# Kernel optimization log

Hardware: AMD Instinct MI355X
Metric: run time of the kernel (lower is better)

## Reference

```python
import jax, jax.numpy as jnp
import numpy as np

D_MODEL = 1024
NUM_HEADS = 16
HEAD_DIM = D_MODEL // NUM_HEADS


def setup_inputs() -> dict:
    key = jax.random.key(0)
    ks = jax.random.split(key, 12)
    B, S = 2, 2048
    scale = 1.0 / np.sqrt(D_MODEL)
    inp = {
        "x": jax.random.normal(ks[0], (B, S, D_MODEL), dtype=jnp.float32),
        "docking_scores": jax.random.uniform(ks[1], (B, S), dtype=jnp.float32),
        "q_w": jax.random.normal(ks[2], (D_MODEL, D_MODEL), dtype=jnp.float32) * scale,
        "q_b": jnp.zeros((D_MODEL,), dtype=jnp.float32),
        "k_w": jax.random.normal(ks[3], (D_MODEL, D_MODEL), dtype=jnp.float32) * scale,
        "k_b": jnp.zeros((D_MODEL,), dtype=jnp.float32),
        "v_w": jax.random.normal(ks[4], (D_MODEL, D_MODEL), dtype=jnp.float32) * scale,
        "v_b": jnp.zeros((D_MODEL,), dtype=jnp.float32),
        "o_w": jax.random.normal(ks[5], (D_MODEL, D_MODEL), dtype=jnp.float32) * scale,
        "o_b": jnp.zeros((D_MODEL,), dtype=jnp.float32),
        "alpha": jnp.float32(0.5),
    }
    return inp


def reference(x, docking_scores, q_w, q_b, k_w, k_b, v_w, v_b, o_w, o_b, alpha):
    B, S, _ = x.shape
    # Projections; weights stored as (in, out) so y = x @ W + b
    def proj(w, b):
        y = jnp.einsum('bsd,de->bse', x, w) + b
        return y.reshape(B, S, NUM_HEADS, HEAD_DIM).transpose(0, 2, 1, 3)  # (B,H,S,hd)
    Q = proj(q_w, q_b)
    K = proj(k_w, k_b)
    V = proj(v_w, v_b)
    scores = jnp.einsum('bhqd,bhkd->bhqk', Q, K) / np.sqrt(HEAD_DIM)
    attn = jax.nn.softmax(scores, axis=-1)  # (B,H,S,S)
    # post-softmax docking blend, broadcast over heads and query positions
    ds = docking_scores[:, None, None, :]  # (B,1,1,S)
    attn = (1.0 - alpha) * attn + alpha * ds
    ctx = jnp.einsum('bhqk,bhkd->bhqd', attn, V)
    ctx = ctx.transpose(0, 2, 1, 3).reshape(B, S, D_MODEL)
    return jnp.einsum('bsd,de->bse', ctx, o_w) + o_b
```

## Files before the change

### kernel.cpp

```cpp
#include <hip/hip_runtime.h>
#include <hip/hip_bf16.h>

typedef __attribute__((ext_vector_type(8)))  short bf16x8;
typedef __attribute__((ext_vector_type(4)))  float f32x4;
typedef __attribute__((ext_vector_type(16))) float f32x16;
typedef __attribute__((ext_vector_type(4)))  int   i32x4;
typedef __attribute__((ext_vector_type(4)))  unsigned short u16x4;
typedef __attribute__((ext_vector_type(8)))  unsigned short u16x8;

__device__ __forceinline__ unsigned short f2bf(float f) {
    unsigned int u = __builtin_bit_cast(unsigned int, f);
    u += 0x7FFFu + ((u >> 16) & 1u);
    return (unsigned short)(u >> 16);
}
__device__ __forceinline__ float bf2f(unsigned short h) {
    unsigned int u = ((unsigned int)h) << 16;
    return __builtin_bit_cast(float, u);
}
__device__ __forceinline__ bf16x8 ld16(const unsigned short* p) {
    return *reinterpret_cast<const bf16x8*>(p);
}
__device__ __forceinline__ float fexp2(float x) {
    float r; asm("v_exp_f32 %0, %1" : "=v"(r) : "v"(x)); return r;
}
__device__ __forceinline__ float frcp(float x) {
    float r; asm("v_rcp_f32 %0, %1" : "=v"(r) : "v"(x)); return r;
}
__device__ __forceinline__ void pswap(unsigned int& a, unsigned int& b) {
    asm("v_permlane32_swap_b32 %0, %1" : "+v"(a), "+v"(b));
}

__global__ void cvt_x_kernel(const float* __restrict__ in, unsigned short* __restrict__ out, int n8) {
    int idx = blockIdx.x * blockDim.x + threadIdx.x;
    int stride = gridDim.x * blockDim.x;
    for (int i = idx; i < n8; i += stride) {
        f32x4 a = reinterpret_cast<const f32x4*>(in)[i*2];
        f32x4 b = reinterpret_cast<const f32x4*>(in)[i*2+1];
        u16x8 o;
        o[0]=f2bf(a[0]); o[1]=f2bf(a[1]); o[2]=f2bf(a[2]); o[3]=f2bf(a[3]);
        o[4]=f2bf(b[0]); o[5]=f2bf(b[1]); o[6]=f2bf(b[2]); o[7]=f2bf(b[3]);
        reinterpret_cast<u16x8*>(out)[i] = o;
    }
}

__global__ void tr_w_kernel(const float* __restrict__ q_w, const float* __restrict__ k_w,
                            const float* __restrict__ v_w, const float* __restrict__ o_w,
                            unsigned short* __restrict__ WT) {
    __shared__ float tile[32][33];
    const float* W = (blockIdx.z == 0) ? q_w : (blockIdx.z == 1) ? k_w : (blockIdx.z == 2) ? v_w : o_w;
    unsigned short* dst = WT + (size_t)blockIdx.z * 1024 * 1024;
    int tx = threadIdx.x, ty = threadIdx.y;
    int n0 = blockIdx.x * 32, k0 = blockIdx.y * 32;
#pragma unroll
    for (int j = 0; j < 4; ++j)
        tile[ty + j*8][tx] = W[(size_t)(k0 + ty + j*8) * 1024 + n0 + tx];
    __syncthreads();
#pragma unroll
    for (int j = 0; j < 4; ++j)
        dst[(size_t)(n0 + ty + j*8) * 1024 + k0 + tx] = f2bf(tile[tx][ty + j*8]);
}


__global__ __launch_bounds__(256) void gemm_qkv(
    const unsigned short* __restrict__ A,
    const unsigned short* __restrict__ WT,
    const float* __restrict__ qb, const float* __restrict__ kbias, const float* __restrict__ vbias,
    unsigned short* __restrict__ Qo, unsigned short* __restrict__ KFo, unsigned short* __restrict__ VFo)
{
    __shared__ __align__(16) unsigned short As[2][128*64];
    __shared__ __align__(16) unsigned short Bs[2][128*64];
    const int tid = threadIdx.x, lane = tid & 63, w = tid >> 6;
    const int wm = w >> 1, wn = w & 1;
    const int m0 = blockIdx.y * 128, n0 = blockIdx.x * 128;
    const int K = 1024;
    const int sr = tid >> 3, ssl = tid & 7;
    const int ssw = (ssl ^ (sr & 7)) << 3;
    f32x4 acc[4][4] = {};

    auto stage = [&](int buf, int k0) {
#pragma unroll
        for (int j = 0; j < 4; ++j) {
            const int c = j*256 + tid, r = j*32 + sr;
            __builtin_amdgcn_global_load_lds(
                (const __attribute__((address_space(1))) void*)&A[(size_t)(m0+r)*K + k0 + ssw],
                (__attribute__((address_space(3))) void*)&As[buf][(size_t)c*8], 16, 0, 0);
            __builtin_amdgcn_global_load_lds(
                (const __attribute__((address_space(1))) void*)&WT[(size_t)(n0+r)*K + k0 + ssw],
                (__attribute__((address_space(3))) void*)&Bs[buf][(size_t)c*8], 16, 0, 0);
        }
    };

    stage(0, 0);
#pragma unroll 1
    for (int t = 0; t < 16; ++t) {
        __syncthreads();
        if (t < 15) stage((t + 1) & 1, (t + 1) * 64);
        const unsigned short* pa = &As[t & 1][0];
        const unsigned short* pb = &Bs[t & 1][0];
#pragma unroll
        for (int kc = 0; kc < 2; ++kc) {
            bf16x8 af[4], bfr[4];
            const int slog = kc*4 + (lane >> 4);
#pragma unroll
            for (int t2 = 0; t2 < 4; ++t2) {
                const int row = wm*64 + t2*16 + (lane & 15);
                af[t2]  = ld16(&pa[row*64 + ((slog ^ (row & 7)) << 3)]);
                const int col = wn*64 + t2*16 + (lane & 15);
                bfr[t2] = ld16(&pb[col*64 + ((slog ^ (col & 7)) << 3)]);
            }
#pragma unroll
            for (int mt = 0; mt < 4; ++mt)
#pragma unroll
                for (int nt = 0; nt < 4; ++nt)
                    acc[mt][nt] = __builtin_amdgcn_mfma_f32_16x16x32_bf16(af[mt], bfr[nt], acc[mt][nt], 0, 0, 0);
        }
    }
    const int mat = n0 >> 10;
    if (mat == 2) {
#pragma unroll
        for (int mt = 0; mt < 4; ++mt)
#pragma unroll
        for (int nt = 0; nt < 4; ++nt) {
            const int nl = (n0 & 1023) + wn*64 + nt*16 + (lane & 15);
            const int h = nl >> 6, hd = nl & 63;
            const int mbase = m0 + wm*64 + mt*16 + ((lane >> 4) << 2);
            const int b = mbase >> 11, s = mbase & 2047;
            const float bv = vbias[nl];
            u16x4 pk;
#pragma unroll
            for (int r = 0; r < 4; ++r) pk[r] = f2bf(acc[mt][nt][r] + bv);
            const size_t off = (size_t)((b << 4) | h) * 131072 + (s >> 6) * 4096 + (hd >> 5) * 2048
                             + ((s >> 4) & 3) * 512 + ((s >> 3) & 1) * 256 + (hd & 31) * 8 + (s & 7);
            *reinterpret_cast<u16x4*>(&VFo[off]) = pk;
        }
    } else if (mat == 1) {
#pragma unroll
        for (int mt = 0; mt < 4; ++mt)
#pragma unroll
        for (int nt = 0; nt < 4; ++nt) {
            const int nl = (n0 & 1023) + wn*64 + nt*16 + (lane & 15);
            const int h = nl >> 6, hd = nl & 63;
            const int mbase = m0 + wm*64 + mt*16 + ((lane >> 4) << 2);
            const float bv = kbias[nl];
#pragma unroll
            for (int r = 0; r < 4; ++r) {
                const int mm2 = mbase + r, b = mm2 >> 11, s = mm2 & 2047;
                const size_t off = (size_t)((b << 4) | h) * 131072 + (s >> 5) * 2048 + (hd >> 4) * 512
                                 + ((hd >> 3) & 1) * 256 + (s & 31) * 8 + (hd & 7);
                KFo[off] = f2bf(acc[mt][nt][r] + bv);
            }
        }
    } else {
        const float scale = 0.180336881f;
#pragma unroll
        for (int mt = 0; mt < 4; ++mt)
#pragma unroll
        for (int nt = 0; nt < 4; ++nt) {
            const int nl = (n0 & 1023) + wn*64 + nt*16 + (lane & 15);
            const int h = nl >> 6, hd = nl & 63;
            const int mbase = m0 + wm*64 + mt*16 + ((lane >> 4) << 2);
            const float bv = qb[nl];
#pragma unroll
            for (int r = 0; r < 4; ++r) {
                const int mm2 = mbase + r, b = mm2 >> 11, s = mm2 & 2047;
                Qo[((size_t)((b << 4) | h) * 2048 + s) * 64 + hd] = f2bf((acc[mt][nt][r] + bv) * scale);
            }
        }
    }
}

__global__ __launch_bounds__(256) void gemm_o(
    const unsigned short* __restrict__ A, const unsigned short* __restrict__ WT,
    const float* __restrict__ bias, float* __restrict__ Cout)
{
    __shared__ __align__(16) unsigned short As[2][128*64];
    __shared__ __align__(16) unsigned short Bs[2][128*64];
    const int tid = threadIdx.x, lane = tid & 63, w = tid >> 6;
    const int wm = w >> 1, wn = w & 1;
    const int m0 = blockIdx.y * 128, n0 = blockIdx.x * 128;
    const int K = 1024;
    const int sr = tid >> 3, ssl = tid & 7;
    const int ssw = (ssl ^ (sr & 7)) << 3;
    f32x4 acc[4][4] = {};

    auto stage = [&](int buf, int k0) {
#pragma unroll
        for (int j = 0; j < 4; ++j) {
            const int c = j*256 + tid, r = j*32 + sr;
            __builtin_amdgcn_global_load_lds(
                (const __attribute__((address_space(1))) void*)&A[(size_t)(m0+r)*K + k0 + ssw],
                (__attribute__((address_space(3))) void*)&As[buf][(size_t)c*8], 16, 0, 0);
            __builtin_amdgcn_global_load_lds(
                (const __attribute__((address_space(1))) void*)&WT[(size_t)(n0+r)*K + k0 + ssw],
                (__attribute__((address_space(3))) void*)&Bs[buf][(size_t)c*8], 16, 0, 0);
        }
    };

    stage(0, 0);
#pragma unroll 1
    for (int t = 0; t < 16; ++t) {
        __syncthreads();
        if (t < 15) stage((t + 1) & 1, (t + 1) * 64);
        const unsigned short* pa = &As[t & 1][0];
        const unsigned short* pb = &Bs[t & 1][0];
#pragma unroll
        for (int kc = 0; kc < 2; ++kc) {
            bf16x8 af[4], bfr[4];
            const int slog = kc*4 + (lane >> 4);
#pragma unroll
            for (int t2 = 0; t2 < 4; ++t2) {
                const int row = wm*64 + t2*16 + (lane & 15);
                af[t2]  = ld16(&pa[row*64 + ((slog ^ (row & 7)) << 3)]);
                const int col = wn*64 + t2*16 + (lane & 15);
                bfr[t2] = ld16(&pb[col*64 + ((slog ^ (col & 7)) << 3)]);
            }
#pragma unroll
            for (int mt = 0; mt < 4; ++mt)
#pragma unroll
                for (int nt = 0; nt < 4; ++nt)
                    acc[mt][nt] = __builtin_amdgcn_mfma_f32_16x16x32_bf16(af[mt], bfr[nt], acc[mt][nt], 0, 0, 0);
        }
    }
#pragma unroll
    for (int mt = 0; mt < 4; ++mt)
#pragma unroll
    for (int nt = 0; nt < 4; ++nt) {
        const int n = n0 + wn*64 + nt*16 + (lane & 15);
        const int mbase = m0 + wm*64 + mt*16 + ((lane >> 4) << 2);
        const float bv = bias[n];
#pragma unroll
        for (int r = 0; r < 4; ++r)
            Cout[(size_t)(mbase + r) * 1024 + n] = acc[mt][nt][r] + bv;
    }
}

__global__ void dock_c_kernel(const float* __restrict__ ds, const unsigned short* __restrict__ VF,
                              float* __restrict__ cvec) {
    __shared__ float red[256];
    const int bh = blockIdx.x;
    const int b = bh >> 4;
    const int t = threadIdx.x;
    const int lane = t & 63, t2 = (t >> 6) & 1, k4 = t >> 7;
    const int hi = lane >> 5;
    const unsigned short* VFb = VF + (size_t)bh * 131072;
    const float* dsb = ds + b * 2048;
    float sum = 0.f;
    for (int kvt = k4; kvt < 32; kvt += 2) {
#pragma unroll
        for (int ks = 0; ks < 4; ++ks) {
            bf16x8 v = ld16(VFb + kvt*4096 + t2*2048 + ks*512 + lane*8);
            const int kv0 = kvt*64 + ks*16 + hi*8;
            f32x4 d0 = *reinterpret_cast<const f32x4*>(&dsb[kv0]);
            f32x4 d1 = *reinterpret_cast<const f32x4*>(&dsb[kv0 + 4]);
            sum += d0[0]*bf2f((unsigned short)v[0]) + d0[1]*bf2f((unsigned short)v[1])
                 + d0[2]*bf2f((unsigned short)v[2]) + d0[3]*bf2f((unsigned short)v[3])
                 + d1[0]*bf2f((unsigned short)v[4]) + d1[1]*bf2f((unsigned short)v[5])
                 + d1[2]*bf2f((unsigned short)v[6]) + d1[3]*bf2f((unsigned short)v[7]);
        }
    }
    red[t] = sum;
    __syncthreads();
    if (t < 64) {
        const int ln = t & 31, tt2 = t >> 5;
        const int base = tt2 * 64 + ln;
        cvec[bh * 64 + tt2 * 32 + ln] = red[base] + red[base + 32] + red[base + 128] + red[base + 160];
    }
}

__global__ __launch_bounds__(256, 2) void attn_kernel(
    const unsigned short* __restrict__ Qp,
    const unsigned short* __restrict__ KF,
    const unsigned short* __restrict__ VF,
    const float* __restrict__ cvec,
    const float* __restrict__ alpha_p,
    unsigned short* __restrict__ ctx)
{
    __shared__ float sml[4][32];
    const int tid = threadIdx.x, lane = tid & 63, w = tid >> 6;
    const int hi = lane >> 5, ln = lane & 31;
    const int wg = blockIdx.x;
    const int swz = (wg & 7) * 64 + (wg >> 3);
    const int bh = swz >> 4, qt = swz & 15;
    const int q0 = qt * 128 + w * 32;
    const size_t hb = (size_t)bh * (2048 * 64);
    const float alpha = *alpha_p;

    const unsigned short* KFb = KF + (size_t)bh * 131072;
    const unsigned short* VFb = VF + (size_t)bh * 131072;

    bf16x8 qf[4];
    {
        const unsigned short* qr = &Qp[hb + (size_t)(q0 + ln) * 64 + hi * 8];
#pragma unroll
        for (int ks = 0; ks < 4; ++ks) qf[ks] = ld16(qr + ks * 16);
    }

    const short one_bf = (short)0x3F80;
    const bf16x8 onesf = {one_bf, one_bf, one_bf, one_bf, one_bf, one_bf, one_bf, one_bf};

    f32x16 oacc0 = {}, oacc1 = {}, lacc = {};
    float m = -1e30f;

    auto ldk = [&](bf16x8 (&kf)[8], int it) {
#pragma unroll
        for (int t2 = 0; t2 < 2; ++t2)
#pragma unroll
        for (int ks = 0; ks < 4; ++ks)
            kf[t2*4+ks] = ld16(KFb + (it*2 + t2)*2048 + ks*512 + lane*8);
    };

    bf16x8 kfA[8], kfB[8];
    ldk(kfA, 0);
    f32x16 sA0 = {}, sA1 = {}, sB0 = {}, sB1 = {};
#pragma unroll
    for (int ks = 0; ks < 4; ++ks) {
        sA0 = __builtin_amdgcn_mfma_f32_32x32x16_bf16(kfA[ks],   qf[ks], sA0, 0, 0, 0);
        sA1 = __builtin_amdgcn_mfma_f32_32x32x16_bf16(kfA[4+ks], qf[ks], sA1, 0, 0, 0);
    }

    auto step = [&](f32x16& sc0, f32x16& sc1, f32x16& sn0, f32x16& sn1, bf16x8 (&kn)[8], int it) {
        bf16x8 vf[8];
#pragma unroll
        for (int t2 = 0; t2 < 2; ++t2)
#pragma unroll
        for (int ks = 0; ks < 4; ++ks)
            vf[t2*4+ks] = ld16(VFb + it*4096 + t2*2048 + ks*512 + lane*8);
        const bool more = (it + 1 < 32);
        if (more) ldk(kn, it + 1);
        float mx[8];
#pragma unroll
        for (int r = 0; r < 8; ++r)
            mx[r] = fmaxf(fmaxf(sc0[r], sc0[r+8]), fmaxf(sc1[r], sc1[r+8]));
        float tm = fmaxf(fmaxf(fmaxf(mx[0],mx[1]), fmaxf(mx[2],mx[3])),
                         fmaxf(fmaxf(mx[4],mx[5]), fmaxf(mx[6],mx[7])));
        {
            unsigned int ua = __builtin_bit_cast(unsigned int, tm), ub = ua;
            pswap(ua, ub);
            tm = fmaxf(__builtin_bit_cast(float, ua), __builtin_bit_cast(float, ub));
        }
        if (__any(tm > m + 8.f)) {
            float mn = fmaxf(m, tm);
            float sc = fexp2(m - mn);
            m = mn;
            if (hi == 0) sml[w][ln] = sc;
#pragma unroll
            for (int m4 = 0; m4 < 4; ++m4) {
                f32x4 sv = *reinterpret_cast<const f32x4*>(&sml[w][m4*8 + hi*4]);
#pragma unroll
                for (int r3 = 0; r3 < 4; ++r3) {
                    oacc0[m4*4+r3] *= sv[r3];
                    oacc1[m4*4+r3] *= sv[r3];
                    lacc [m4*4+r3] *= sv[r3];
                }
            }
        }
        float p0a[16], p1a[16];
#pragma unroll
        for (int r = 0; r < 16; ++r) {
            p0a[r] = fexp2(sc0[r] - m);
            p1a[r] = fexp2(sc1[r] - m);
        }
        unsigned int Wp0[4][2], Wp1[4][2];
#pragma unroll
        for (int m4 = 0; m4 < 4; ++m4)
#pragma unroll
        for (int jj = 0; jj < 2; ++jj) {
            asm("v_cvt_pk_bf16_f32 %0, %1, %2" : "=v"(Wp0[m4][jj]) : "v"(p0a[m4*4+jj*2]), "v"(p0a[m4*4+jj*2+1]));
            asm("v_cvt_pk_bf16_f32 %0, %1, %2" : "=v"(Wp1[m4][jj]) : "v"(p1a[m4*4+jj*2]), "v"(p1a[m4*4+jj*2+1]));
        }
        __builtin_amdgcn_s_setprio(1);
        if (more) {
            sn0 = {}; sn1 = {};
#pragma unroll
            for (int ks = 0; ks < 4; ++ks) {
                sn0 = __builtin_amdgcn_mfma_f32_32x32x16_bf16(kn[ks],   qf[ks], sn0, 0, 0, 0);
                sn1 = __builtin_amdgcn_mfma_f32_32x32x16_bf16(kn[4+ks], qf[ks], sn1, 0, 0, 0);
            }
        }
#pragma unroll
        for (int ks = 0; ks < 4; ++ks) {
            const int tp = ks & 1;
            unsigned int a0, a1, b0, b1;
            if (ks < 2) { a0 = Wp0[2*tp][0]; a1 = Wp0[2*tp][1]; b0 = Wp0[2*tp+1][0]; b1 = Wp0[2*tp+1][1]; }
            else        { a0 = Wp1[2*tp][0]; a1 = Wp1[2*tp][1]; b0 = Wp1[2*tp+1][0]; b1 = Wp1[2*tp+1][1]; }
            pswap(a0, b0);
            pswap(a1, b1);
            i32x4 pw;
            pw[0] = (int)a0; pw[1] = (int)a1; pw[2] = (int)b0; pw[3] = (int)b1;
            bf16x8 pf = __builtin_bit_cast(bf16x8, pw);
            oacc0 = __builtin_amdgcn_mfma_f32_32x32x16_bf16(pf, vf[ks],   oacc0, 0, 0, 0);
            oacc1 = __builtin_amdgcn_mfma_f32_32x32x16_bf16(pf, vf[4+ks], oacc1, 0, 0, 0);
            lacc  = __builtin_amdgcn_mfma_f32_32x32x16_bf16(pf, onesf,    lacc,  0, 0, 0);
        }
        __builtin_amdgcn_s_setprio(0);
    };

#pragma unroll 1
    for (int ii = 0; ii < 16; ++ii) {
        step(sA0, sA1, sB0, sB1, kfB, ii*2);
        step(sB0, sB1, sA0, sA1, kfA, ii*2 + 1);
    }

    const int b = bh >> 4, h = bh & 15;
    const float a1f = 1.f - alpha;
    const float cv0 = alpha * cvec[bh*64 + ln];
    const float cv1 = alpha * cvec[bh*64 + 32 + ln];
#pragma unroll
    for (int m4 = 0; m4 < 4; ++m4) {
#pragma unroll
        for (int r3 = 0; r3 < 4; ++r3) {
            const int row = m4*8 + hi*4 + r3;
            const int s = q0 + row;
            const float iv = frcp(lacc[m4*4 + r3]);
            unsigned short* orow = &ctx[((size_t)(b*2048 + s))*1024 + h*64 + ln];
            orow[0]  = f2bf(a1f * oacc0[m4*4+r3] * iv + cv0);
            orow[32] = f2bf(a1f * oacc1[m4*4+r3] * iv + cv1);
        }
    }
}

extern "C" void kernel_launch(void* const* d_in, const int* in_sizes, int n_in,
                              void* d_out, int out_size, void* d_ws, size_t ws_size,
                              hipStream_t stream) {
    const float* x     = (const float*)d_in[0];
    const float* ds    = (const float*)d_in[1];
    const float* q_w   = (const float*)d_in[2];
    const float* q_b   = (const float*)d_in[3];
    const float* k_w   = (const float*)d_in[4];
    const float* k_b   = (const float*)d_in[5];
    const float* v_w   = (const float*)d_in[6];
    const float* v_b   = (const float*)d_in[7];
    const float* o_w   = (const float*)d_in[8];
    const float* o_b   = (const float*)d_in[9];
    const float* alpha = (const float*)d_in[10];

    char* ws = (char*)d_ws;
    const size_t MB = 1024 * 1024;
    unsigned short* xb   = (unsigned short*)(ws);
    unsigned short* wT   = (unsigned short*)(ws + 8  * MB);
    unsigned short* Qb   = (unsigned short*)(ws + 16 * MB);
    unsigned short* KFb  = (unsigned short*)(ws + 24 * MB);
    unsigned short* VFb  = (unsigned short*)(ws + 32 * MB);
    float*          cvec = (float*)         (ws + 40 * MB);
    unsigned short* ctxb = xb;

    const int M = 4096, K = 1024;

    cvt_x_kernel<<<2048, 256, 0, stream>>>(x, xb, M * K / 8);

    dim3 tb(32, 8);
    dim3 tg(32, 32, 4);
    tr_w_kernel<<<tg, tb, 0, stream>>>(q_w, k_w, v_w, o_w, wT);

    dim3 gqkv(24, 32);
    gemm_qkv<<<gqkv, 256, 0, stream>>>(xb, wT, q_b, k_b, v_b, Qb, KFb, VFb);

    dock_c_kernel<<<32, 256, 0, stream>>>(ds, VFb, cvec);

    attn_kernel<<<512, 256, 0, stream>>>(Qb, KFb, VFb, cvec, alpha, ctxb);

    dim3 go(8, 32);
    gemm_o<<<go, 256, 0, stream>>>(ctxb, wT + (size_t)3 * MB, o_b, (float*)d_out);
}
```

Baseline: 141.7 us.

## Stage K/V tiles through double-buffered LDS with direct global-to-LDS loads

Before this change, each of the four waves in a block loaded the same K and V tiles from global memory on its own. Now the block loads each tile once, using global_load_lds, into two LDS buffers (one filling while the other is read), and the waves read their fragments from LDS. This cuts redundant global and L2 traffic by about four times. The next tile's QK MFMAs are also moved ahead of the softmax max/exp work so they overlap with it. The cost is a block-wide __syncthreads every step and 32 KB of extra LDS, which may hurt wave independence and occupancy.

```diff
diff --git a/kernel.cpp b/kernel.cpp
--- a/kernel.cpp
+++ b/kernel.cpp
@@ -275,6 +275,8 @@
     const float* __restrict__ alpha_p,
     unsigned short* __restrict__ ctx)
 {
+    __shared__ __align__(16) unsigned short Ks[2][4096];
+    __shared__ __align__(16) unsigned short Vs[2][4096];
     __shared__ float sml[4][32];
     const int tid = threadIdx.x, lane = tid & 63, w = tid >> 6;
     const int hi = lane >> 5, ln = lane & 31;
@@ -287,6 +289,7 @@
 
     const unsigned short* KFb = KF + (size_t)bh * 131072;
     const unsigned short* VFb = VF + (size_t)bh * 131072;
+    const int fo = lane * 8;
 
     bf16x8 qf[4];
     {
@@ -301,32 +304,58 @@
     f32x16 oacc0 = {}, oacc1 = {}, lacc = {};
     float m = -1e30f;
 
-    auto ldk = [&](bf16x8 (&kf)[8], int it) {
+    auto stage = [&](int buf, int it) {
+#pragma unroll
+        for (int p = 0; p < 2; ++p) {
+            __builtin_amdgcn_global_load_lds(
+                (const __attribute__((address_space(1))) void*)(KFb + it*4096 + p*2048 + tid*8),
+                (__attribute__((address_space(3))) void*)&Ks[buf][p*2048 + tid*8], 16, 0, 0);
+            __builtin_amdgcn_global_load_lds(
+                (const __attribute__((address_space(1))) void*)(VFb + it*4096 + p*2048 + tid*8),
+                (__attribute__((address_space(3))) void*)&Vs[buf][p*2048 + tid*8], 16, 0, 0);
+        }
+    };
+
+    bf16x8 kf[8];
+    auto ldk = [&](const unsigned short* base) {
 #pragma unroll
         for (int t2 = 0; t2 < 2; ++t2)
 #pragma unroll
         for (int ks = 0; ks < 4; ++ks)
-            kf[t2*4+ks] = ld16(KFb + (it*2 + t2)*2048 + ks*512 + lane*8);
+            kf[t2*4+ks] = ld16(base + t2*2048 + ks*512 + fo);
     };
 
-    bf16x8 kfA[8], kfB[8];
-    ldk(kfA, 0);
+    stage(0, 0);
+    __syncthreads();
+    stage(1, 1);
+    ldk(&Ks[0][0]);
     f32x16 sA0 = {}, sA1 = {}, sB0 = {}, sB1 = {};
 #pragma unroll
     for (int ks = 0; ks < 4; ++ks) {
-        sA0 = __builtin_amdgcn_mfma_f32_32x32x16_bf16(kfA[ks],   qf[ks], sA0, 0, 0, 0);
-        sA1 = __builtin_amdgcn_mfma_f32_32x32x16_bf16(kfA[4+ks], qf[ks], sA1, 0, 0, 0);
-    }
-
-    auto step = [&](f32x16& sc0, f32x16& sc1, f32x16& sn0, f32x16& sn1, bf16x8 (&kn)[8], int it) {
+        sA0 = __builtin_amdgcn_mfma_f32_32x32x16_bf16(kf[ks],   qf[ks], sA0, 0, 0, 0);
+        sA1 = __builtin_amdgcn_mfma_f32_32x32x16_bf16(kf[4+ks], qf[ks], sA1, 0, 0, 0);
+    }
+
+    auto step = [&](f32x16& sc0, f32x16& sc1, f32x16& sn0, f32x16& sn1, int buf, int it) {
         bf16x8 vf[8];
 #pragma unroll
         for (int t2 = 0; t2 < 2; ++t2)
 #pragma unroll
         for (int ks = 0; ks < 4; ++ks)
-            vf[t2*4+ks] = ld16(VFb + it*4096 + t2*2048 + ks*512 + lane*8);
+            vf[t2*4+ks] = ld16(&Vs[buf][t2*2048 + ks*512 + fo]);
+        __syncthreads();
+        if (it + 2 < 32) stage(buf, it + 2);
         const bool more = (it + 1 < 32);
-        if (more) ldk(kn, it + 1);
+        if (more) ldk(&Ks[buf ^ 1][0]);
+        __builtin_amdgcn_s_setprio(1);
+        if (more) {
+            sn0 = {}; sn1 = {};
+#pragma unroll
+            for (int ks = 0; ks < 4; ++ks) {
+                sn0 = __builtin_amdgcn_mfma_f32_32x32x16_bf16(kf[ks],   qf[ks], sn0, 0, 0, 0);
+                sn1 = __builtin_amdgcn_mfma_f32_32x32x16_bf16(kf[4+ks], qf[ks], sn1, 0, 0, 0);
+            }
+        }
         float mx[8];
 #pragma unroll
         for (int r = 0; r < 8; ++r)
@@ -360,6 +389,7 @@
             p0a[r] = fexp2(sc0[r] - m);
             p1a[r] = fexp2(sc1[r] - m);
         }
+
         unsigned int Wp0[4][2], Wp1[4][2];
 #pragma unroll
         for (int m4 = 0; m4 < 4; ++m4)
@@ -367,15 +397,6 @@
         for (int jj = 0; jj < 2; ++jj) {
             asm("v_cvt_pk_bf16_f32 %0, %1, %2" : "=v"(Wp0[m4][jj]) : "v"(p0a[m4*4+jj*2]), "v"(p0a[m4*4+jj*2+1]));
             asm("v_cvt_pk_bf16_f32 %0, %1, %2" : "=v"(Wp1[m4][jj]) : "v"(p1a[m4*4+jj*2]), "v"(p1a[m4*4+jj*2+1]));
-        }
-        __builtin_amdgcn_s_setprio(1);
-        if (more) {
-            sn0 = {}; sn1 = {};
-#pragma unroll
-            for (int ks = 0; ks < 4; ++ks) {
-                sn0 = __builtin_amdgcn_mfma_f32_32x32x16_bf16(kn[ks],   qf[ks], sn0, 0, 0, 0);
-                sn1 = __builtin_amdgcn_mfma_f32_32x32x16_bf16(kn[4+ks], qf[ks], sn1, 0, 0, 0);
-            }
         }
 #pragma unroll
         for (int ks = 0; ks < 4; ++ks) {
@@ -397,8 +418,8 @@
 
 #pragma unroll 1
     for (int ii = 0; ii < 16; ++ii) {
-        step(sA0, sA1, sB0, sB1, kfB, ii*2);
-        step(sB0, sB1, sA0, sA1, kfA, ii*2 + 1);
+        step(sA0, sA1, sB0, sB1, 0, ii*2);
+        step(sB0, sB1, sA0, sA1, 1, ii*2 + 1);
     }
 
     const int b = bh >> 4, h = bh & 15;
```

Result: faster. 132.6 us (-6.4%).
